# Optimization experiments

Hardware: AMD Instinct MI355X
Metric: run time of the kernel (lower is better)

Reference implementation:

```python
import jax, jax.numpy as jnp
import numpy as np

E, T, IN, OUT, GS = 8, 2048, 2048, 2048, 64


def setup_inputs() -> dict:
    key = jax.random.key(0)
    k1, k2, k3, k4, k5 = jax.random.split(key, 5)
    x = jax.random.normal(k1, (T, IN), dtype=jnp.float32)
    # int4 codes in [0,16): stored unpacked as int32 for the reference
    qweight = jax.random.randint(k2, (E, IN, OUT), 0, 16, dtype=jnp.int32)
    G = IN // GS  # quant groups along the reduction dim
    scales = jax.random.uniform(k3, (E, G, OUT), jnp.float32, minval=0.005, maxval=0.02)
    zeros = jax.random.normal(k4, (E, G, OUT), jnp.float32) * 0.01
    scales_and_zeros = jnp.stack([scales, zeros], axis=-1)  # [E, G, OUT, 2]
    # tokens sorted by expert: per-expert counts are diffs of sorted cut points, sum == T
    cuts = jnp.sort(jax.random.randint(k5, (E - 1,), 0, T + 1, dtype=jnp.int32))
    bounds = jnp.concatenate([jnp.zeros((1,), jnp.int32), cuts, jnp.full((1,), T, jnp.int32)])
    tokens_per_expert = jnp.diff(bounds).astype(jnp.int32)  # [E]
    return {
        "x": x,
        "qweight": qweight,
        "scales_and_zeros": scales_and_zeros,
        "tokens_per_expert": tokens_per_expert,
        "group_size": GS,
    }


def reference(x, qweight, scales_and_zeros, tokens_per_expert, group_size):
    """Grouped (per-expert) int4 dequant + GEMM over an expert-sorted token matrix.

    Math of aten._weight_int4pack_mm per expert e over each quant group g:
        W_e[k, n] = (q_e[k, n] - 8) * scale_e[g, n] + zero_e[g, n],  g = k // group_size
        out[rows_e] = x[rows_e] @ W_e
    where rows_e is the contiguous slice given by cumsum(tokens_per_expert).
    """
    n_exp, in_f, out_f = qweight.shape
    n_tok = x.shape[0]
    G = in_f // group_size

    # dequantize all expert weights: [E, IN, OUT]
    q = qweight.reshape(n_exp, G, group_size, out_f).astype(x.dtype)
    scales = scales_and_zeros[..., 0][:, :, None, :]  # [E, G, 1, OUT]
    zeros = scales_and_zeros[..., 1][:, :, None, :]   # [E, G, 1, OUT]
    W = ((q - 8.0) * scales + zeros).reshape(n_exp, in_f, out_f)

    # expert id per token from the cumsum boundaries (tokens are expert-sorted)
    cum = jnp.cumsum(tokens_per_expert)                                # [E]
    eid = jnp.searchsorted(cum, jnp.arange(n_tok), side="right")       # [T]
    onehot = (eid[:, None] == jnp.arange(n_exp)[None, :]).astype(x.dtype)  # [T, E]

    # dispatch -> per-expert GEMM -> combine (jit-safe grouped GEMM)
    xe = jnp.einsum("te,ti->eti", onehot, x)       # [E, T, IN]
    ye = jnp.einsum("eti,eio->eto", xe, W)         # [E, T, OUT]
    out = jnp.einsum("te,eto->to", onehot, ye)     # [T, OUT]
    return out
```

## Files before the change

### kernel.cpp

```cpp
#include <hip/hip_runtime.h>
#include <hip/hip_bf16.h>

constexpr int NE  = 8;
constexpr int T   = 2048;
constexpr int IN  = 2048;
constexpr int OUT = 2048;
constexpr int GS  = 64;
constexpr int G   = IN / GS;

constexpr int BM = 128;
constexpr int BN = 64;
constexpr int BK = 64;
constexpr int NTILE = IN / BK;
constexpr int LDB = 64;
constexpr int MAXMT = T / BM + NE;

using short8  = __attribute__((ext_vector_type(8))) short;
using short4v = __attribute__((ext_vector_type(4))) short;
using floatx4 = __attribute__((ext_vector_type(4))) float;
using int4v   = __attribute__((ext_vector_type(4))) int;
using float4v = __attribute__((ext_vector_type(4))) float;

__global__ __launch_bounds__(256)
void cvt_x_bf16(const float* __restrict__ x, __hip_bfloat16* __restrict__ xb) {
    const int i = (blockIdx.x * 256 + threadIdx.x) * 4;
    const float4 v = *(const float4*)(x + i);
    union { unsigned long long u; __hip_bfloat162 h2[2]; } p;
    p.h2[0] = __float22bfloat162_rn(float2{v.x, v.y});
    p.h2[1] = __float22bfloat162_rn(float2{v.z, v.w});
    *(unsigned long long*)(xb + i) = p.u;
}

__global__ __launch_bounds__(256, 3)
void hqq_grouped_gemm(const __hip_bfloat16* __restrict__ xb,
                      const int*   __restrict__ qw,
                      const float* __restrict__ snz,
                      const int*   __restrict__ tpe,
                      float* __restrict__ out) {
    const int tid = threadIdx.x;
    const int n0  = blockIdx.x * BN;

    const int mt = blockIdx.y;
    int e = -1, b0 = 0, b1 = 0, tm = 0;
    {
        int base = 0, rem = mt;
#pragma unroll
        for (int i = 0; i < NE; ++i) {
            const int c  = tpe[i];
            const int nt = (c + BM - 1) >> 7;
            if (e < 0) {
                if (rem < nt) { e = i; b0 = base; b1 = base + c; tm = rem; }
                else rem -= nt;
            }
            base += c;
        }
    }
    if (e < 0) return;
    const int row0 = b0 + tm * BM;

    __shared__ __hip_bfloat16 Bs[2][BN][LDB];

    floatx4 acc[2][4];
#pragma unroll
    for (int i = 0; i < 2; ++i)
#pragma unroll
        for (int j = 0; j < 4; ++j)
            acc[i][j] = (floatx4){0.f, 0.f, 0.f, 0.f};

    const int n4  = (tid & 15) * 4;
    const int kq4 = (tid >> 4) * 4;
    const int wsz = (tid & 3) << 4;

    const int lane = tid & 63;
    const int wid  = tid >> 6;
    const int wm = wid * 32;
    const int lm = lane & 15;
    const int lk = (lane >> 4) * 8;
    const int rsz = ((lm >> 2) & 3) << 4;

    const int*    qbase  = qw + (size_t)e * IN * OUT + n0 + n4;
    const float2* szbase = (const float2*)snz + (size_t)e * G * OUT + n0 + n4;

    const int r0c = min(row0 + wm + lm,      b1 - 1);
    const int r1c = min(row0 + wm + 16 + lm, b1 - 1);
    const __hip_bfloat16* ap0 = xb + (size_t)r0c * IN + lk;
    const __hip_bfloat16* ap1 = xb + (size_t)r1c * IN + lk;

    int4v   qvX[4], qvY[4];
    float4v szX[2], szY[2];
    short8  afA[4], afB[4];

#define GLOAD16(dst, addr) \
    asm volatile("global_load_dwordx4 %0, %1, off" : "=v"(dst) : "v"(addr))
#define GLOAD16_OFF(dst, addr, B) \
    asm volatile("global_load_dwordx4 %0, %1, off offset:" #B : "=v"(dst) : "v"(addr))

    auto issue_q = [&](int t, int4v (&qv)[4], float4v (&sz)[2]) {
        const int k0 = t * BK;
        const float4v* szp = (const float4v*)(szbase + (size_t)(k0 >> 6) * OUT);
        GLOAD16(sz[0], szp);
        GLOAD16_OFF(sz[1], szp, 16);
#pragma unroll
        for (int kk = 0; kk < 4; ++kk) {
            const int* qp = qbase + (size_t)(k0 + kq4 + kk) * OUT;
            GLOAD16(qv[kk], qp);
        }
    };

    auto issue_af = [&](int t, short8 (&af)[4]) {
        const __hip_bfloat16* p0 = ap0 + t * BK;
        const __hip_bfloat16* p1 = ap1 + t * BK;
        GLOAD16(af[0], p0);
        GLOAD16(af[1], p1);
        GLOAD16_OFF(af[2], p0, 64);
        GLOAD16_OFF(af[3], p1, 64);
    };

    auto stage = [&](__hip_bfloat16 (&B)[BN][LDB], int4v (&qv)[4], float4v (&sz)[2]) {
#pragma unroll
        for (int nn = 0; nn < 4; ++nn) {
            const float sc = sz[nn >> 1][(nn & 1) * 2];
            const float cc = sz[nn >> 1][(nn & 1) * 2 + 1] - 8.0f * sc;
            union { short4v v; __hip_bfloat162 h2[2]; } pb;
            pb.h2[0] = __float22bfloat162_rn(float2{(float)qv[0][nn] * sc + cc,
                                                    (float)qv[1][nn] * sc + cc});
            pb.h2[1] = __float22bfloat162_rn(float2{(float)qv[2][nn] * sc + cc,
                                                    (float)qv[3][nn] * sc + cc});
            *(short4v*)&B[n4 + nn][kq4 ^ wsz] = pb.v;
        }
    };

    auto mfma_tile = [&](const __hip_bfloat16 (&B)[BN][LDB], const short8 (&af)[4]) {
#pragma unroll
        for (int ks2 = 0; ks2 < 2; ++ks2) {
            short8 bfr[4];
#pragma unroll
            for (int j = 0; j < 4; ++j)
                bfr[j] = *(const short8*)&B[j * 16 + lm][(ks2 * 32 + lk) ^ rsz];
#pragma unroll
            for (int i = 0; i < 2; ++i)
#pragma unroll
                for (int j = 0; j < 4; ++j)
                    acc[i][j] = __builtin_amdgcn_mfma_f32_16x16x32_bf16(
                        af[ks2 * 2 + i], bfr[j], acc[i][j], 0, 0, 0);
        }
    };

#define PHASE(TT, QS, AS, BB, WA, WE)                                   \
    asm volatile("s_waitcnt vmcnt(" #WA ")" ::: "memory");              \
    __builtin_amdgcn_sched_barrier(0);                                  \
    stage(Bs[BB], qv##QS, sz##QS);                                      \
    issue_q((TT) + 2 < NTILE ? (TT) + 2 : NTILE - 1, qv##QS, sz##QS);   \
    asm volatile("s_waitcnt lgkmcnt(0)" ::: "memory");                  \
    __builtin_amdgcn_s_barrier();                                       \
    __builtin_amdgcn_sched_barrier(0);                                  \
    asm volatile("s_waitcnt vmcnt(" #WE ")" ::: "memory");              \
    __builtin_amdgcn_sched_barrier(0);                                  \
    mfma_tile(Bs[BB], af##AS);                                          \
    issue_af((TT) + 2 < NTILE ? (TT) + 2 : NTILE - 1, af##AS);

    issue_q(0, qvX, szX);
    issue_q(1, qvY, szY);
    issue_af(0, afA);
    issue_af(1, afB);

    PHASE(0, X, A, 0, 14, 10)
    PHASE(1, Y, B, 1, 18, 16)
    for (int it = 0; it < 15; ++it) {
        const int t = 2 + it * 2;
        PHASE(t,     X, A, 0, 14, 16)
        PHASE(t + 1, Y, B, 1, 14, 16)
    }
#undef PHASE
#undef GLOAD16
#undef GLOAD16_OFF

    const int lq = (lane >> 4) * 4;
#pragma unroll
    for (int i = 0; i < 2; ++i) {
#pragma unroll
        for (int r = 0; r < 4; ++r) {
            const int row = row0 + wm + i * 16 + lq + r;
            if (row < b1) {
                float* op = out + (size_t)row * OUT + n0 + lm;
#pragma unroll
                for (int j = 0; j < 4; ++j)
                    op[j * 16] = acc[i][j][r];
            }
        }
    }
}

extern "C" void kernel_launch(void* const* d_in, const int* in_sizes, int n_in,
                              void* d_out, int out_size, void* d_ws, size_t ws_size,
                              hipStream_t stream) {
    const float* x   = (const float*)d_in[0];
    const int*   qw  = (const int*)d_in[1];
    const float* snz = (const float*)d_in[2];
    const int*   tpe = (const int*)d_in[3];
    float* out = (float*)d_out;
    __hip_bfloat16* xb = (__hip_bfloat16*)d_ws;

    cvt_x_bf16<<<(T * IN) / (256 * 4), 256, 0, stream>>>(x, xb);

    dim3 grid(OUT / BN, MAXMT, 1);
    hqq_grouped_gemm<<<grid, 256, 0, stream>>>(xb, qw, snz, tpe, out);
}
```

Measured before the change: 248.3 us.

## Split K reduction across two 256-thread chains per block with LDS combine

Doubles the block to 512 threads, with each half computing the same output tile over half of the reduction dimension using its own double-buffered LDS slice. At the end, the second chain writes its partial accumulators to LDS and the first chain adds them before storing. This halves the serial K loop per wave to expose more memory parallelism. The cost is a larger LDS footprint per block, an extra reduction pass through LDS, and shared block-wide barriers between the two chains.

```diff
diff --git a/kernel.cpp b/kernel.cpp
--- a/kernel.cpp
+++ b/kernel.cpp
@@ -12,6 +12,7 @@
 constexpr int BN = 64;
 constexpr int BK = 64;
 constexpr int NTILE = IN / BK;
+constexpr int HT  = NTILE / 2;
 constexpr int LDB = 64;
 constexpr int MAXMT = T / BM + NE;
 
@@ -31,7 +32,7 @@
     *(unsigned long long*)(xb + i) = p.u;
 }
 
-__global__ __launch_bounds__(256, 3)
+__global__ __launch_bounds__(512, 2)
 void hqq_grouped_gemm(const __hip_bfloat16* __restrict__ xb,
                       const int*   __restrict__ qw,
                       const float* __restrict__ snz,
@@ -58,7 +59,7 @@
     if (e < 0) return;
     const int row0 = b0 + tm * BM;
 
-    __shared__ __hip_bfloat16 Bs[2][BN][LDB];
+    __shared__ __hip_bfloat16 Bs[2][2][BN][LDB];
 
     floatx4 acc[2][4];
 #pragma unroll
@@ -67,15 +68,18 @@
         for (int j = 0; j < 4; ++j)
             acc[i][j] = (floatx4){0.f, 0.f, 0.f, 0.f};
 
-    const int n4  = (tid & 15) * 4;
-    const int kq4 = (tid >> 4) * 4;
-    const int wsz = (tid & 3) << 4;
-
-    const int lane = tid & 63;
-    const int wid  = tid >> 6;
-    const int wm = wid * 32;
-    const int lm = lane & 15;
-    const int lk = (lane >> 4) * 8;
+    const int ct    = tid & 255;
+    const int chain = tid >> 8;
+    const int lane  = tid & 63;
+    const int cwid  = (tid >> 6) & 3;
+
+    const int n4  = (ct & 15) * 4;
+    const int kq4 = ((ct >> 4) & 15) * 4;
+    const int wsz = (ct & 3) << 4;
+
+    const int wm  = cwid * 32;
+    const int lm  = lane & 15;
+    const int hi  = lane >> 4;
     const int rsz = ((lm >> 2) & 3) << 4;
 
     const int*    qbase  = qw + (size_t)e * IN * OUT + n0 + n4;
@@ -83,8 +87,11 @@
 
     const int r0c = min(row0 + wm + lm,      b1 - 1);
     const int r1c = min(row0 + wm + 16 + lm, b1 - 1);
-    const __hip_bfloat16* ap0 = xb + (size_t)r0c * IN + lk;
-    const __hip_bfloat16* ap1 = xb + (size_t)r1c * IN + lk;
+    const __hip_bfloat16* ap0 = xb + (size_t)r0c * IN + (hi * 8);
+    const __hip_bfloat16* ap1 = xb + (size_t)r1c * IN + (hi * 8);
+
+    const int tb = chain * HT;
+    const int tl = tb + HT - 1;
 
     int4v   qvX[4], qvY[4];
     float4v szX[2], szY[2];
@@ -136,7 +143,7 @@
             short8 bfr[4];
 #pragma unroll
             for (int j = 0; j < 4; ++j)
-                bfr[j] = *(const short8*)&B[j * 16 + lm][(ks2 * 32 + lk) ^ rsz];
+                bfr[j] = *(const short8*)&B[j * 16 + lm][(ks2 * 32 + hi * 8) ^ rsz];
 #pragma unroll
             for (int i = 0; i < 2; ++i)
 #pragma unroll
@@ -146,46 +153,62 @@
         }
     };
 
-#define PHASE(TT, QS, AS, BB, WA, WE)                                   \
+#define PHASE(LL, QS, AS, BB, WA, WE)                                   \
     asm volatile("s_waitcnt vmcnt(" #WA ")" ::: "memory");              \
     __builtin_amdgcn_sched_barrier(0);                                  \
-    stage(Bs[BB], qv##QS, sz##QS);                                      \
-    issue_q((TT) + 2 < NTILE ? (TT) + 2 : NTILE - 1, qv##QS, sz##QS);   \
+    stage(Bs[chain][BB], qv##QS, sz##QS);                               \
+    issue_q((LL) + 2 < HT ? tb + (LL) + 2 : tl, qv##QS, sz##QS);        \
     asm volatile("s_waitcnt lgkmcnt(0)" ::: "memory");                  \
     __builtin_amdgcn_s_barrier();                                       \
     __builtin_amdgcn_sched_barrier(0);                                  \
     asm volatile("s_waitcnt vmcnt(" #WE ")" ::: "memory");              \
     __builtin_amdgcn_sched_barrier(0);                                  \
-    mfma_tile(Bs[BB], af##AS);                                          \
-    issue_af((TT) + 2 < NTILE ? (TT) + 2 : NTILE - 1, af##AS);
-
-    issue_q(0, qvX, szX);
-    issue_q(1, qvY, szY);
-    issue_af(0, afA);
-    issue_af(1, afB);
+    mfma_tile(Bs[chain][BB], af##AS);                                   \
+    issue_af((LL) + 2 < HT ? tb + (LL) + 2 : tl, af##AS);
+
+    issue_q(tb,     qvX, szX);
+    issue_q(tb + 1, qvY, szY);
+    issue_af(tb,     afA);
+    issue_af(tb + 1, afB);
 
     PHASE(0, X, A, 0, 14, 10)
     PHASE(1, Y, B, 1, 18, 16)
-    for (int it = 0; it < 15; ++it) {
-        const int t = 2 + it * 2;
-        PHASE(t,     X, A, 0, 14, 16)
-        PHASE(t + 1, Y, B, 1, 14, 16)
+    for (int it = 0; it < 7; ++it) {
+        const int p = 2 + it * 2;
+        PHASE(p,     X, A, 0, 14, 16)
+        PHASE(p + 1, Y, B, 1, 14, 16)
     }
 #undef PHASE
 #undef GLOAD16
 #undef GLOAD16_OFF
 
-    const int lq = (lane >> 4) * 4;
-#pragma unroll
-    for (int i = 0; i < 2; ++i) {
-#pragma unroll
-        for (int r = 0; r < 4; ++r) {
-            const int row = row0 + wm + i * 16 + lq + r;
-            if (row < b1) {
-                float* op = out + (size_t)row * OUT + n0 + lm;
-#pragma unroll
-                for (int j = 0; j < 4; ++j)
-                    op[j * 16] = acc[i][j][r];
+    __syncthreads();
+    float* cbuf = (float*)&Bs[0][0][0][0];
+    if (chain == 1) {
+#pragma unroll
+        for (int i = 0; i < 2; ++i)
+#pragma unroll
+            for (int j = 0; j < 4; ++j)
+#pragma unroll
+                for (int r = 0; r < 4; ++r)
+                    cbuf[((i * 4 + j) * 4 + r) * 256 + cwid * 64 + lane] = acc[i][j][r];
+    }
+    __syncthreads();
+
+    if (chain == 0) {
+        const int lq = hi * 4;
+#pragma unroll
+        for (int i = 0; i < 2; ++i) {
+#pragma unroll
+            for (int r = 0; r < 4; ++r) {
+                const int row = row0 + wm + i * 16 + lq + r;
+                if (row < b1) {
+                    float* op = out + (size_t)row * OUT + n0 + lm;
+#pragma unroll
+                    for (int j = 0; j < 4; ++j)
+                        op[j * 16] = acc[i][j][r]
+                                   + cbuf[((i * 4 + j) * 4 + r) * 256 + cwid * 64 + lane];
+                }
             }
         }
     }
@@ -204,5 +227,5 @@
     cvt_x_bf16<<<(T * IN) / (256 * 4), 256, 0, stream>>>(x, xb);
 
     dim3 grid(OUT / BN, MAXMT, 1);
-    hqq_grouped_gemm<<<grid, 256, 0, stream>>>(xb, qw, snz, tpe, out);
+    hqq_grouped_gemm<<<grid, 512, 0, stream>>>(xb, qw, snz, tpe, out);
 }
```

Result: no change. 244.9 us (-1.4%).
